# Optimization experiments

Measured on AMD Instinct MI355X. Metric: run time of the kernel, lower is better.

Reference implementation:

```python
import jax, jax.numpy as jnp
import numpy as np

B, S_SRC, S_TGT = 32, 128, 128
V, E, H = 32000, 256, 256
PAD_ID = 0
NEG = -1.0e9


def setup_inputs() -> dict:
    key = jax.random.key(0)
    ks = jax.random.split(key, 16)
    lengths_de = jax.random.randint(ks[0], (B,), S_SRC // 2, S_SRC + 1)
    idx_de = jax.random.randint(ks[1], (B, S_SRC), 1, V)
    pos = jnp.arange(S_SRC)[None, :]
    indices_de = jnp.where(pos < lengths_de[:, None], idx_de, PAD_ID)
    indices_en = jax.random.randint(ks[2], (B, S_TGT), 1, V)
    lengths_en = jnp.full((B,), S_TGT, dtype=jnp.int32)

    sc = 0.02
    def nrm(k, shape):
        return jax.random.normal(k, shape, dtype=jnp.float32) * sc
    emb_enc = nrm(ks[3], (V, E)).at[PAD_ID].set(0.0)
    emb_dec = nrm(ks[4], (V, E)).at[PAD_ID].set(0.0)
    return {
        "indices_de": indices_de, "lengths_de": lengths_de,
        "indices_en": indices_en, "lengths_en": lengths_en,
        "emb_enc": emb_enc, "emb_dec": emb_dec,
        "W_ih_enc": nrm(ks[5], (H, E)), "W_hh_enc": nrm(ks[6], (H, H)),
        "b_ih_enc": jnp.zeros((H,), jnp.float32), "b_hh_enc": jnp.zeros((H,), jnp.float32),
        "W_ih_dec": nrm(ks[7], (H, E)), "W_hh_dec": nrm(ks[8], (H, H)),
        "b_ih_dec": jnp.zeros((H,), jnp.float32), "b_hh_dec": jnp.zeros((H,), jnp.float32),
        "W_attn": nrm(ks[9], (H, 2 * H)), "b_attn": jnp.zeros((H,), jnp.float32),
        "W_out": nrm(ks[10], (V, H)), "b_out": jnp.zeros((V,), jnp.float32),
    }


def reference(indices_de, lengths_de, indices_en, lengths_en,
              emb_enc, emb_dec,
              W_ih_enc, W_hh_enc, b_ih_enc, b_hh_enc,
              W_ih_dec, W_hh_dec, b_ih_dec, b_hh_dec,
              W_attn, b_attn, W_out, b_out):
    # ---- Encoder: tanh RNN over packed sequence ----
    x_enc = emb_enc[indices_de]                      # [B, S, E]
    valid = jnp.arange(S_SRC)[None, :] < lengths_de[:, None]  # [B, S]

    def enc_step(h, inp):
        x_t, v_t = inp                                # [B,E], [B]
        h_new = jnp.tanh(x_t @ W_ih_enc.T + b_ih_enc + h @ W_hh_enc.T + b_hh_enc)
        h = jnp.where(v_t[:, None], h_new, h)         # frozen past length (pack semantics)
        out = jnp.where(v_t[:, None], h_new, 0.0)     # padded outputs are zero
        return h, out

    h0 = jnp.zeros((B, H), jnp.float32)
    h_final, enc_outs = jax.lax.scan(
        enc_step, h0, (x_enc.transpose(1, 0, 2), valid.T))
    encoder_outputs = enc_outs.transpose(1, 0, 2)     # [B, S, H]
    enc_mask = indices_de == PAD_ID                   # [B, S] True at padding

    # ---- Decoder: per-step RNN cell + dot-product attention + vocab proj ----
    x_dec = emb_dec[indices_en]                       # [B, T, E]

    def dec_step(h, x_t):
        h = jnp.tanh(x_t @ W_ih_dec.T + b_ih_dec + h @ W_hh_dec.T + b_hh_dec)
        scores = jnp.einsum('bh,bsh->bs', h, encoder_outputs)
        scores = jnp.where(enc_mask, NEG, scores)
        attn = jax.nn.softmax(scores, axis=-1)
        context = jnp.einsum('bs,bsh->bh', attn, encoder_outputs)
        combined = jnp.concatenate([context, h], axis=1)          # [B, 2H]
        attn_out = jnp.tanh(combined @ W_attn.T + b_attn)         # [B, H]
        logits_t = attn_out @ W_out.T + b_out                     # [B, V]
        return h, logits_t

    _, logits = jax.lax.scan(dec_step, h_final, x_dec.transpose(1, 0, 2))
    return logits.transpose(1, 0, 2)                  # [B, T, V]
```

## Files before the change

### kernel.cpp

```cpp
#include <hip/hip_runtime.h>
#include <stdint.h>

#define B_ 32
#define S_ 128
#define T_ 128
#define V_ 32000
#define E_ 256
#define H_ 256
#define NEG_ (-1.0e9f)

typedef __attribute__((ext_vector_type(8))) short short8;
typedef __attribute__((ext_vector_type(4))) float floatx4;

__device__ __forceinline__ unsigned short f2bf(float x){
  unsigned u = __float_as_uint(x);
  u = u + 0x7fffu + ((u >> 16) & 1u);
  return (unsigned short)(u >> 16);
}
__device__ __forceinline__ float bf2f(unsigned short s){
  return __uint_as_float(((unsigned)s) << 16);
}
__device__ __forceinline__ float hsum4(float4 v){ return (v.x+v.y)+(v.z+v.w); }
__device__ __forceinline__ void unpack8(uint4 q, float4& lo, float4& hi){
  lo.x = __uint_as_float(q.x << 16); lo.y = __uint_as_float(q.x & 0xffff0000u);
  lo.z = __uint_as_float(q.y << 16); lo.w = __uint_as_float(q.y & 0xffff0000u);
  hi.x = __uint_as_float(q.z << 16); hi.y = __uint_as_float(q.z & 0xffff0000u);
  hi.z = __uint_as_float(q.w << 16); hi.w = __uint_as_float(q.w & 0xffff0000u);
}

#define GLOAD_LDS16(gptr, lptr) \
  __builtin_amdgcn_global_load_lds( \
      (const __attribute__((address_space(1))) unsigned int*)(const void*)(gptr), \
      (__attribute__((address_space(3))) unsigned int*)(void*)(lptr), 16, 0, 0)

#define LDS_BARRIER() do { \
    asm volatile("s_waitcnt lgkmcnt(0)" ::: "memory"); \
    __builtin_amdgcn_s_barrier(); \
  } while(0)

__device__ __forceinline__ void cvt_body(const float* __restrict__ src,
                                         unsigned short* __restrict__ dst,
                                         int blk, int n4){
  int i = blk*256 + (int)threadIdx.x;
  if (i < n4){
    float4 v = ((const float4*)src)[i];
    ushort4 o; o.x=f2bf(v.x); o.y=f2bf(v.y); o.z=f2bf(v.z); o.w=f2bf(v.w);
    ((ushort4*)dst)[i] = o;
  }
}

__device__ __forceinline__ void xih_body(
    const int* __restrict__ idxmat, const float* __restrict__ emb,
    const float* __restrict__ Wih,
    const float* __restrict__ b1, const float* __restrict__ b2,
    float* __restrict__ out, int blk,
    int* idx_s, float4 (*x_s)[64])
{
  int b = blk >> 3;
  int t0 = (blk & 7) << 4;
  int tid = threadIdx.x;
  if (tid < 16) idx_s[tid] = idxmat[b*128 + t0 + tid];
  __syncthreads();
  for (int r = 0; r < 16; ++r)
    ((float*)&x_s[r][0])[tid] = emb[(size_t)idx_s[r]*E_ + tid];
  __syncthreads();
  int j2 = tid & 127, tg = tid >> 7;
  const float4* W0 = (const float4*)(Wih + (size_t)j2*E_);
  const float4* W1 = (const float4*)(Wih + (size_t)(j2+128)*E_);
  float4 a0[8], a1[8];
  #pragma unroll
  for (int t=0;t<8;++t){ a0[t]={0,0,0,0}; a1[t]={0,0,0,0}; }
  for (int e4 = 0; e4 < 64; ++e4){
    float4 w0 = W0[e4], w1 = W1[e4];
    #pragma unroll
    for (int t = 0; t < 8; ++t){
      float4 xv = x_s[tg*8+t][e4];
      a0[t] += w0*xv; a1[t] += w1*xv;
    }
  }
  float bi0 = b1[j2] + b2[j2];
  float bi1 = b1[j2+128] + b2[j2+128];
  #pragma unroll
  for (int t = 0; t < 8; ++t){
    size_t row = (size_t)((b<<7) + t0 + tg*8 + t)*H_;
    out[row + j2]     = hsum4(a0[t]) + bi0;
    out[row + j2+128] = hsum4(a1[t]) + bi1;
  }
}

__global__ __launch_bounds__(256) void k_prep(
    const float* __restrict__ W_out, unsigned short* __restrict__ Wout_bf,
    const float* __restrict__ W_attn, unsigned short* __restrict__ Wattn_bf,
    const int* __restrict__ indices_de, const float* __restrict__ emb_enc,
    const float* __restrict__ W_ih_enc, const float* __restrict__ b_ih_enc,
    const float* __restrict__ b_hh_enc, float* __restrict__ Xih_enc,
    const int* __restrict__ indices_en, const float* __restrict__ emb_dec,
    const float* __restrict__ W_ih_dec, const float* __restrict__ b_ih_dec,
    const float* __restrict__ b_hh_dec, float* __restrict__ Xih_dec)
{
  __shared__ int idx_s[16];
  __shared__ float4 x_s[16][64];
  int bx = blockIdx.x;
  if (bx < 8000){
    cvt_body(W_out, Wout_bf, bx, 2048000);
  } else if (bx < 8128){
    cvt_body(W_attn, Wattn_bf, bx - 8000, 32768);
  } else if (bx < 8384){
    xih_body(indices_de, emb_enc, W_ih_enc, b_ih_enc, b_hh_enc, Xih_enc,
             bx - 8128, idx_s, x_s);
  } else {
    xih_body(indices_en, emb_dec, W_ih_dec, b_ih_dec, b_hh_dec, Xih_dec,
             bx - 8384, idx_s, x_s);
  }
}

__global__ __launch_bounds__(512, 2) void k_rnn2(
    const float* __restrict__ Whh_e, const float* __restrict__ Whh_d,
    const float* __restrict__ Xih_e, const float* __restrict__ Xih_d,
    const int* __restrict__ lengths,
    unsigned short* __restrict__ enc_out,
    float* __restrict__ hseq)
{
  __shared__ float h_s[256];
  __shared__ float part[8][256];
  int b = blockIdx.x, tid = threadIdx.x;
  int kk = tid >> 6;
  int jg = tid & 63;
  float4 w[4][8];
  #pragma unroll
  for (int r = 0; r < 4; ++r){
    const float4* Wr = (const float4*)(Whh_e + (size_t)(jg + (r<<6))*H_ + (kk<<5));
    #pragma unroll
    for (int i = 0; i < 8; ++i) w[r][i] = Wr[i];
  }
  if (tid < 256) h_s[tid] = 0.f;
  int len = lengths[b];
  __syncthreads();

  for (int t = 0; t < 128; ++t){
    float x = 0.f;
    if (tid < 256) x = Xih_e[(size_t)((b<<7) + t)*H_ + tid];
    const float4* h4 = ((const float4*)h_s) + (kk << 3);
    float4 hv[8];
    #pragma unroll
    for (int i = 0; i < 8; ++i) hv[i] = h4[i];
    #pragma unroll
    for (int r = 0; r < 4; ++r){
      float4 a = {0,0,0,0};
      #pragma unroll
      for (int i = 0; i < 8; ++i) a += w[r][i]*hv[i];
      part[kk][jg + (r<<6)] = hsum4(a);
    }
    LDS_BARRIER();
    if (tid < 256){
      float s = x;
      #pragma unroll
      for (int q = 0; q < 8; ++q) s += part[q][tid];
      float hn = tanhf(s);
      float hold = h_s[tid];
      bool v = (t < len);
      h_s[tid] = v ? hn : hold;
      enc_out[(size_t)((b<<7)+t)*H_ + tid] = f2bf(v ? hn : 0.f);
    }
    LDS_BARRIER();
  }

  #pragma unroll
  for (int r = 0; r < 4; ++r){
    const float4* Wr = (const float4*)(Whh_d + (size_t)(jg + (r<<6))*H_ + (kk<<5));
    #pragma unroll
    for (int i = 0; i < 8; ++i) w[r][i] = Wr[i];
  }
  for (int t = 0; t < 128; ++t){
    float x = 0.f;
    if (tid < 256) x = Xih_d[(size_t)((b<<7) + t)*H_ + tid];
    const float4* h4 = ((const float4*)h_s) + (kk << 3);
    float4 hv[8];
    #pragma unroll
    for (int i = 0; i < 8; ++i) hv[i] = h4[i];
    #pragma unroll
    for (int r = 0; r < 4; ++r){
      float4 a = {0,0,0,0};
      #pragma unroll
      for (int i = 0; i < 8; ++i) a += w[r][i]*hv[i];
      part[kk][jg + (r<<6)] = hsum4(a);
    }
    LDS_BARRIER();
    if (tid < 256){
      float s = x;
      #pragma unroll
      for (int q = 0; q < 8; ++q) s += part[q][tid];
      float hn = tanhf(s);
      h_s[tid] = hn;
      hseq[(size_t)((b<<7)+t)*H_ + tid] = hn;
    }
    LDS_BARRIER();
  }
}

__global__ __launch_bounds__(256) void k_attn(
    const unsigned short* __restrict__ enc_out,
    const float* __restrict__ hseq,
    const int* __restrict__ lengths,
    const unsigned short* __restrict__ Wattn,
    const float* __restrict__ battn,
    unsigned short* __restrict__ attn_out)
{
  __shared__ float h_sm[16][256];
  __shared__ float sc[16][132];
  __shared__ float comb[16][512];
  int bx = blockIdx.x; int b = bx >> 3; int t0 = (bx & 7) << 4;
  int tid = threadIdx.x;
  int len = lengths[b];
  for (int r = 0; r < 16; ++r)
    h_sm[r][tid] = hseq[(size_t)((b<<7) + t0 + r)*H_ + tid];
  __syncthreads();
  {
    int s = tid & 127, tg = tid >> 7;
    float4 a[8];
    #pragma unroll
    for (int t=0;t<8;++t) a[t] = {0,0,0,0};
    const uint4* ep = (const uint4*)(enc_out + (size_t)(b*S_ + s)*H_);
    for (int oct = 0; oct < 32; ++oct){
      uint4 q = ep[oct];
      float4 elo, ehi; unpack8(q, elo, ehi);
      #pragma unroll
      for (int t = 0; t < 8; ++t){
        const float4* hp = (const float4*)&h_sm[tg*8+t][oct*8];
        a[t] += elo*hp[0] + ehi*hp[1];
      }
    }
    #pragma unroll
    for (int t = 0; t < 8; ++t)
      sc[tg*8+t][s] = (s < len) ? hsum4(a[t]) : NEG_;
  }
  __syncthreads();
  {
    int wv = tid >> 6, ln = tid & 63;
    for (int r = 0; r < 4; ++r){
      int t = r*4 + wv;
      float v0 = sc[t][ln], v1 = sc[t][ln+64];
      float m = fmaxf(v0, v1);
      #pragma unroll
      for (int off = 32; off >= 1; off >>= 1) m = fmaxf(m, __shfl_xor(m, off));
      float e0 = __expf(v0 - m), e1 = __expf(v1 - m);
      float su = e0 + e1;
      #pragma unroll
      for (int off = 32; off >= 1; off >>= 1) su += __shfl_xor(su, off);
      float inv = 1.0f / su;
      sc[t][ln] = e0*inv; sc[t][ln+64] = e1*inv;
    }
  }
  __syncthreads();
  {
    int hd = tid & 127, tg = tid >> 7;
    float c0[8], c1[8];
    #pragma unroll
    for (int t=0;t<8;++t){ c0[t]=0.f; c1[t]=0.f; }
    for (int s4 = 0; s4 < 32; ++s4){
      float ea[4], eb[4];
      #pragma unroll
      for (int i = 0; i < 4; ++i){
        const unsigned short* er = enc_out + (size_t)(b*S_ + s4*4 + i)*H_;
        ea[i] = bf2f(er[hd]); eb[i] = bf2f(er[hd+128]);
      }
      #pragma unroll
      for (int t = 0; t < 8; ++t){
        float4 av = *(const float4*)&sc[tg*8+t][s4*4];
        c0[t] += av.x*ea[0] + av.y*ea[1] + av.z*ea[2] + av.w*ea[3];
        c1[t] += av.x*eb[0] + av.y*eb[1] + av.z*eb[2] + av.w*eb[3];
      }
    }
    #pragma unroll
    for (int t = 0; t < 8; ++t){
      comb[tg*8+t][hd]     = c0[t];
      comb[tg*8+t][hd+128] = c1[t];
    }
  }
  for (int r = 0; r < 16; ++r) comb[r][256 + tid] = h_sm[r][tid];
  __syncthreads();
  {
    int j2 = tid & 127, tg = tid >> 7;
    float4 a0[8], a1[8];
    #pragma unroll
    for (int t=0;t<8;++t){ a0[t]={0,0,0,0}; a1[t]={0,0,0,0}; }
    const uint4* W0 = (const uint4*)(Wattn + (size_t)j2*512);
    const uint4* W1 = (const uint4*)(Wattn + (size_t)(j2+128)*512);
    for (int oct = 0; oct < 64; ++oct){
      float4 w0lo, w0hi, w1lo, w1hi;
      unpack8(W0[oct], w0lo, w0hi);
      unpack8(W1[oct], w1lo, w1hi);
      #pragma unroll
      for (int t = 0; t < 8; ++t){
        const float4* cp = (const float4*)&comb[tg*8+t][oct*8];
        float4 clo = cp[0], chi = cp[1];
        a0[t] += w0lo*clo + w0hi*chi;
        a1[t] += w1lo*clo + w1hi*chi;
      }
    }
    float bi0 = battn[j2], bi1 = battn[j2+128];
    #pragma unroll
    for (int t = 0; t < 8; ++t){
      size_t row = (size_t)((b<<7) + t0 + tg*8 + t)*H_;
      attn_out[row + j2]     = f2bf(tanhf(hsum4(a0[t]) + bi0));
      attn_out[row + j2+128] = f2bf(tanhf(hsum4(a1[t]) + bi1));
    }
  }
}

#define VB_STAGE(bufi, s) do { \
    _Pragma("unroll") \
    for (int i_ = 0; i_ < 4; ++i_){ \
      int c_ = tid + i_*512; \
      int r_ = c_ >> 5; \
      int sc_ = (c_ & 31) ^ (r_ & 7); \
      GLOAD_LDS16(Wb + (size_t)(ncol0 + (s)*64 + r_)*256 + sc_*8, \
                  &Bsm[bufi][c_*8]); \
    } \
  } while(0)

#define VB_STEP(s, Wlit, DOSTAGE) do { \
    asm volatile("s_waitcnt vmcnt(" Wlit ")" ::: "memory"); \
    __builtin_amdgcn_s_barrier(); \
    floatx4 acc[2][4]; \
    _Pragma("unroll") \
    for (int mi=0;mi<2;++mi) \
      _Pragma("unroll") \
      for (int ni=0;ni<4;++ni) acc[mi][ni]=(floatx4){0.f,0.f,0.f,0.f}; \
    _Pragma("unroll") \
    for (int k0=0;k0<8;++k0){ \
      short8 bfr[4]; \
      _Pragma("unroll") \
      for (int ni=0;ni<4;++ni) \
        bfr[ni] = *(const short8*)&Bsm[(s)&1][(ni*16+llo)*256 + (((k0*4+lhi)^(llo&7))<<3)]; \
      _Pragma("unroll") \
      for (int ni=0;ni<4;++ni){ \
        acc[0][ni] = __builtin_amdgcn_mfma_f32_16x16x32_bf16(af[0][k0], bfr[ni], acc[0][ni], 0,0,0); \
        acc[1][ni] = __builtin_amdgcn_mfma_f32_16x16x32_bf16(af[1][k0], bfr[ni], acc[1][ni], 0,0,0); \
      } \
    } \
    asm volatile("s_waitcnt lgkmcnt(0)" ::: "memory"); \
    __builtin_amdgcn_s_barrier(); \
    _Pragma("unroll") \
    for (int ni=0;ni<4;++ni){ \
      int col_ = ncol0 + (s)*64 + ni*16 + llo; \
      _Pragma("unroll") \
      for (int mi=0;mi<2;++mi){ \
        _Pragma("unroll") \
        for (int r_=0;r_<4;++r_){ \
          int row_ = mrow0 + mi*16 + lhi*4 + r_; \
          out[(size_t)row_*V_ + col_] = acc[mi][ni][r_] + bpre[s][ni]; \
        } \
      } \
    } \
    asm volatile("" ::: "memory"); \
    if (DOSTAGE) VB_STAGE((s)&1, (s)+2); \
    asm volatile("" ::: "memory"); \
  } while(0)

__global__ __launch_bounds__(512) void k_vocab(
    const unsigned short* __restrict__ A,
    const unsigned short* __restrict__ Wb,
    const float* __restrict__ bout,
    float* __restrict__ out)
{
  __shared__ alignas(16) unsigned short Bsm[2][64*256];
  int bid = blockIdx.x;
  int xcd = bid & 7;
  int gid = xcd*250 + (bid >> 3);
  int mb = gid / 125, ng = gid % 125;
  int tid = threadIdx.x;
  int ln  = tid & 63;
  int w   = tid >> 6;
  int llo = ln & 15, lhi = ln >> 4;
  int mrow0 = mb*256 + w*32;
  int ncol0 = ng*256;

  short8 af[2][8];
  #pragma unroll
  for (int mi=0;mi<2;++mi)
    #pragma unroll
    for (int k0=0;k0<8;++k0)
      af[mi][k0] = *(const short8*)(A + (size_t)(mrow0 + mi*16 + llo)*256 + k0*32 + lhi*8);
  float bpre[4][4];
  #pragma unroll
  for (int s=0;s<4;++s)
    #pragma unroll
    for (int ni=0;ni<4;++ni)
      bpre[s][ni] = bout[ncol0 + s*64 + ni*16 + llo];

  VB_STAGE(0, 0);
  VB_STAGE(1, 1);

  VB_STEP(0, "4",  1);
  VB_STEP(1, "36", 1);
  VB_STEP(2, "36", 0);
  VB_STEP(3, "32", 0);
}

extern "C" void kernel_launch(void* const* d_in, const int* in_sizes, int n_in,
                              void* d_out, int out_size, void* d_ws, size_t ws_size,
                              hipStream_t stream){
  const int*   indices_de = (const int*)d_in[0];
  const int*   lengths_de = (const int*)d_in[1];
  const int*   indices_en = (const int*)d_in[2];
  const float* emb_enc   = (const float*)d_in[4];
  const float* emb_dec   = (const float*)d_in[5];
  const float* W_ih_enc  = (const float*)d_in[6];
  const float* W_hh_enc  = (const float*)d_in[7];
  const float* b_ih_enc  = (const float*)d_in[8];
  const float* b_hh_enc  = (const float*)d_in[9];
  const float* W_ih_dec  = (const float*)d_in[10];
  const float* W_hh_dec  = (const float*)d_in[11];
  const float* b_ih_dec  = (const float*)d_in[12];
  const float* b_hh_dec  = (const float*)d_in[13];
  const float* W_attn    = (const float*)d_in[14];
  const float* b_attn    = (const float*)d_in[15];
  const float* W_out     = (const float*)d_in[16];
  const float* b_out     = (const float*)d_in[17];

  char* ws = (char*)d_ws;
  size_t o = 0;
  float* Xih_enc = (float*)(ws + o); o += (size_t)4096*256*4;
  float* Xih_dec = (float*)(ws + o); o += (size_t)4096*256*4;
  unsigned short* enc_bf = (unsigned short*)(ws + o); o += (size_t)4096*256*2;
  float* hdec    = (float*)(ws + o); o += (size_t)4096*256*4;
  unsigned short* attn_o  = (unsigned short*)(ws + o); o += (size_t)4096*256*2;
  unsigned short* Wout_bf = (unsigned short*)(ws + o); o += (size_t)V_*256*2;
  unsigned short* Wattn_bf= (unsigned short*)(ws + o); o += (size_t)256*512*2;

  k_prep<<<8640, 256, 0, stream>>>(
      W_out, Wout_bf, W_attn, Wattn_bf,
      indices_de, emb_enc, W_ih_enc, b_ih_enc, b_hh_enc, Xih_enc,
      indices_en, emb_dec, W_ih_dec, b_ih_dec, b_hh_dec, Xih_dec);
  k_rnn2<<<32, 512, 0, stream>>>(W_hh_enc, W_hh_dec, Xih_enc, Xih_dec,
                                 lengths_de, enc_bf, hdec);
  k_attn<<<256, 256, 0, stream>>>(enc_bf, hdec, lengths_de, Wattn_bf, b_attn, attn_o);
  k_vocab<<<2000, 512, 0, stream>>>(attn_o, Wout_bf, b_out, (float*)d_out);
}
```

Before: 943.9 us.

## Overlap weight bf16 conversion with serial RNN and vectorize vocab stores

Moves the W_out and W_attn fp32-to-bf16 conversion out of the prep kernel and into extra blocks of the RNN kernel. The 32 latency-bound recurrence blocks then run alongside the bandwidth-bound conversion instead of after it. The RNN inner loops are changed so each thread owns four contiguous output rows and writes its partial sums and h as vectors. The vocab GEMM swaps the MFMA operands so each lane holds four consecutive columns, which allows float4 output and bias accesses, and the vmcnt waits are adjusted to the new store count. The risk is that the conversion blocks compete with the recurrence blocks for CU time or bandwidth.

```diff
diff --git a/kernel.cpp b/kernel.cpp
--- a/kernel.cpp
+++ b/kernel.cpp
@@ -37,17 +37,6 @@
     asm volatile("s_waitcnt lgkmcnt(0)" ::: "memory"); \
     __builtin_amdgcn_s_barrier(); \
   } while(0)
-
-__device__ __forceinline__ void cvt_body(const float* __restrict__ src,
-                                         unsigned short* __restrict__ dst,
-                                         int blk, int n4){
-  int i = blk*256 + (int)threadIdx.x;
-  if (i < n4){
-    float4 v = ((const float4*)src)[i];
-    ushort4 o; o.x=f2bf(v.x); o.y=f2bf(v.y); o.z=f2bf(v.z); o.w=f2bf(v.w);
-    ((ushort4*)dst)[i] = o;
-  }
-}
 
 __device__ __forceinline__ void xih_body(
     const int* __restrict__ idxmat, const float* __restrict__ emb,
@@ -88,9 +77,7 @@
   }
 }
 
-__global__ __launch_bounds__(256) void k_prep(
-    const float* __restrict__ W_out, unsigned short* __restrict__ Wout_bf,
-    const float* __restrict__ W_attn, unsigned short* __restrict__ Wattn_bf,
+__global__ __launch_bounds__(256) void k_xih(
     const int* __restrict__ indices_de, const float* __restrict__ emb_enc,
     const float* __restrict__ W_ih_enc, const float* __restrict__ b_ih_enc,
     const float* __restrict__ b_hh_enc, float* __restrict__ Xih_enc,
@@ -101,35 +88,48 @@
   __shared__ int idx_s[16];
   __shared__ float4 x_s[16][64];
   int bx = blockIdx.x;
-  if (bx < 8000){
-    cvt_body(W_out, Wout_bf, bx, 2048000);
-  } else if (bx < 8128){
-    cvt_body(W_attn, Wattn_bf, bx - 8000, 32768);
-  } else if (bx < 8384){
+  if (bx < 256)
     xih_body(indices_de, emb_enc, W_ih_enc, b_ih_enc, b_hh_enc, Xih_enc,
-             bx - 8128, idx_s, x_s);
-  } else {
+             bx, idx_s, x_s);
+  else
     xih_body(indices_en, emb_dec, W_ih_dec, b_ih_dec, b_hh_dec, Xih_dec,
-             bx - 8384, idx_s, x_s);
-  }
-}
-
-__global__ __launch_bounds__(512, 2) void k_rnn2(
+             bx - 256, idx_s, x_s);
+}
+
+__global__ __launch_bounds__(512, 1) void k_rnnfused(
     const float* __restrict__ Whh_e, const float* __restrict__ Whh_d,
     const float* __restrict__ Xih_e, const float* __restrict__ Xih_d,
     const int* __restrict__ lengths,
     unsigned short* __restrict__ enc_out,
-    float* __restrict__ hseq)
+    float* __restrict__ hseq,
+    const float* __restrict__ W_out, unsigned short* __restrict__ Wout_bf,
+    const float* __restrict__ W_attn, unsigned short* __restrict__ Wattn_bf)
 {
-  __shared__ float h_s[256];
-  __shared__ float part[8][256];
-  int b = blockIdx.x, tid = threadIdx.x;
+  int bx = blockIdx.x;
+  int tid = threadIdx.x;
+  if (bx >= 32){
+    int cb = bx - 32;
+    const float* src; unsigned short* dst; int n4;
+    if (cb < 4000){ src = W_out; dst = Wout_bf; n4 = 2048000; }
+    else          { src = W_attn; dst = Wattn_bf; n4 = 32768; cb -= 4000; }
+    int i = cb*512 + tid;
+    if (i < n4){
+      float4 v = ((const float4*)src)[i];
+      ushort4 o; o.x=f2bf(v.x); o.y=f2bf(v.y); o.z=f2bf(v.z); o.w=f2bf(v.w);
+      ((ushort4*)dst)[i] = o;
+    }
+    return;
+  }
+  __shared__ alignas(16) float h_s[256];
+  __shared__ alignas(16) float part[8][256];
+  int b = bx;
   int kk = tid >> 6;
   int jg = tid & 63;
+  int j0 = jg << 2;
   float4 w[4][8];
   #pragma unroll
   for (int r = 0; r < 4; ++r){
-    const float4* Wr = (const float4*)(Whh_e + (size_t)(jg + (r<<6))*H_ + (kk<<5));
+    const float4* Wr = (const float4*)(Whh_e + (size_t)(j0 + r)*H_ + (kk<<5));
     #pragma unroll
     for (int i = 0; i < 8; ++i) w[r][i] = Wr[i];
   }
@@ -138,61 +138,77 @@
   __syncthreads();
 
   for (int t = 0; t < 128; ++t){
-    float x = 0.f;
-    if (tid < 256) x = Xih_e[(size_t)((b<<7) + t)*H_ + tid];
+    float2 x2 = {0.f, 0.f};
+    if (tid < 128) x2 = *(const float2*)&Xih_e[(size_t)((b<<7) + t)*H_ + tid*2];
     const float4* h4 = ((const float4*)h_s) + (kk << 3);
     float4 hv[8];
     #pragma unroll
     for (int i = 0; i < 8; ++i) hv[i] = h4[i];
-    #pragma unroll
-    for (int r = 0; r < 4; ++r){
-      float4 a = {0,0,0,0};
-      #pragma unroll
-      for (int i = 0; i < 8; ++i) a += w[r][i]*hv[i];
-      part[kk][jg + (r<<6)] = hsum4(a);
-    }
+    float4 pr;
+    {
+      float4 a0={0,0,0,0}, a1={0,0,0,0}, a2={0,0,0,0}, a3={0,0,0,0};
+      #pragma unroll
+      for (int i = 0; i < 8; ++i){
+        a0 += w[0][i]*hv[i]; a1 += w[1][i]*hv[i];
+        a2 += w[2][i]*hv[i]; a3 += w[3][i]*hv[i];
+      }
+      pr.x = hsum4(a0); pr.y = hsum4(a1); pr.z = hsum4(a2); pr.w = hsum4(a3);
+    }
+    *(float4*)&part[kk][j0] = pr;
     LDS_BARRIER();
-    if (tid < 256){
-      float s = x;
-      #pragma unroll
-      for (int q = 0; q < 8; ++q) s += part[q][tid];
-      float hn = tanhf(s);
-      float hold = h_s[tid];
+    if (tid < 128){
+      float s0 = x2.x, s1 = x2.y;
+      #pragma unroll
+      for (int q = 0; q < 8; ++q){
+        float2 p = *(const float2*)&part[q][tid*2];
+        s0 += p.x; s1 += p.y;
+      }
+      float hn0 = tanhf(s0), hn1 = tanhf(s1);
+      float2 old = *(const float2*)&h_s[tid*2];
       bool v = (t < len);
-      h_s[tid] = v ? hn : hold;
-      enc_out[(size_t)((b<<7)+t)*H_ + tid] = f2bf(v ? hn : 0.f);
+      float2 nh; nh.x = v ? hn0 : old.x; nh.y = v ? hn1 : old.y;
+      *(float2*)&h_s[tid*2] = nh;
+      ushort2 ob; ob.x = f2bf(v ? hn0 : 0.f); ob.y = f2bf(v ? hn1 : 0.f);
+      *(ushort2*)&enc_out[(size_t)((b<<7)+t)*H_ + tid*2] = ob;
     }
     LDS_BARRIER();
   }
 
   #pragma unroll
   for (int r = 0; r < 4; ++r){
-    const float4* Wr = (const float4*)(Whh_d + (size_t)(jg + (r<<6))*H_ + (kk<<5));
+    const float4* Wr = (const float4*)(Whh_d + (size_t)(j0 + r)*H_ + (kk<<5));
     #pragma unroll
     for (int i = 0; i < 8; ++i) w[r][i] = Wr[i];
   }
   for (int t = 0; t < 128; ++t){
-    float x = 0.f;
-    if (tid < 256) x = Xih_d[(size_t)((b<<7) + t)*H_ + tid];
+    float2 x2 = {0.f, 0.f};
+    if (tid < 128) x2 = *(const float2*)&Xih_d[(size_t)((b<<7) + t)*H_ + tid*2];
     const float4* h4 = ((const float4*)h_s) + (kk << 3);
     float4 hv[8];
     #pragma unroll
     for (int i = 0; i < 8; ++i) hv[i] = h4[i];
-    #pragma unroll
-    for (int r = 0; r < 4; ++r){
-      float4 a = {0,0,0,0};
-      #pragma unroll
-      for (int i = 0; i < 8; ++i) a += w[r][i]*hv[i];
-      part[kk][jg + (r<<6)] = hsum4(a);
-    }
+    float4 pr;
+    {
+      float4 a0={0,0,0,0}, a1={0,0,0,0}, a2={0,0,0,0}, a3={0,0,0,0};
+      #pragma unroll
+      for (int i = 0; i < 8; ++i){
+        a0 += w[0][i]*hv[i]; a1 += w[1][i]*hv[i];
+        a2 += w[2][i]*hv[i]; a3 += w[3][i]*hv[i];
+      }
+      pr.x = hsum4(a0); pr.y = hsum4(a1); pr.z = hsum4(a2); pr.w = hsum4(a3);
+    }
+    *(float4*)&part[kk][j0] = pr;
     LDS_BARRIER();
-    if (tid < 256){
-      float s = x;
-      #pragma unroll
-      for (int q = 0; q < 8; ++q) s += part[q][tid];
-      float hn = tanhf(s);
-      h_s[tid] = hn;
-      hseq[(size_t)((b<<7)+t)*H_ + tid] = hn;
+    if (tid < 128){
+      float s0 = x2.x, s1 = x2.y;
+      #pragma unroll
+      for (int q = 0; q < 8; ++q){
+        float2 p = *(const float2*)&part[q][tid*2];
+        s0 += p.x; s1 += p.y;
+      }
+      float hn0 = tanhf(s0), hn1 = tanhf(s1);
+      *(float2*)&h_s[tid*2] = (float2){hn0, hn1};
+      *(float2*)&hseq[(size_t)((b<<7)+t)*H_ + tid*2] = (float2){hn0, hn1};
     }
     LDS_BARRIER();
   }
@@ -335,22 +351,24 @@
         bfr[ni] = *(const short8*)&Bsm[(s)&1][(ni*16+llo)*256 + (((k0*4+lhi)^(llo&7))<<3)]; \
       _Pragma("unroll") \
       for (int ni=0;ni<4;++ni){ \
-        acc[0][ni] = __builtin_amdgcn_mfma_f32_16x16x32_bf16(af[0][k0], bfr[ni], acc[0][ni], 0,0,0); \
-        acc[1][ni] = __builtin_amdgcn_mfma_f32_16x16x32_bf16(af[1][k0], bfr[ni], acc[1][ni], 0,0,0); \
+        acc[0][ni] = __builtin_amdgcn_mfma_f32_16x16x32_bf16(bfr[ni], af[0][k0], acc[0][ni], 0,0,0); \
+        acc[1][ni] = __builtin_amdgcn_mfma_f32_16x16x32_bf16(bfr[ni], af[1][k0], acc[1][ni], 0,0,0); \
       } \
     } \
     asm volatile("s_waitcnt lgkmcnt(0)" ::: "memory"); \
     __builtin_amdgcn_s_barrier(); \
     _Pragma("unroll") \
     for (int ni=0;ni<4;++ni){ \
-      int col_ = ncol0 + (s)*64 + ni*16 + llo; \
+      int col_ = ncol0 + (s)*64 + ni*16 + (lhi<<2); \
       _Pragma("unroll") \
       for (int mi=0;mi<2;++mi){ \
-        _Pragma("unroll") \
-        for (int r_=0;r_<4;++r_){ \
-          int row_ = mrow0 + mi*16 + lhi*4 + r_; \
-          out[(size_t)row_*V_ + col_] = acc[mi][ni][r_] + bpre[s][ni]; \
-        } \
+        int row_ = mrow0 + mi*16 + llo; \
+        float4 o_; \
+        o_.x = acc[mi][ni][0] + bpre4[s][ni].x; \
+        o_.y = acc[mi][ni][1] + bpre4[s][ni].y; \
+        o_.z = acc[mi][ni][2] + bpre4[s][ni].z; \
+        o_.w = acc[mi][ni][3] + bpre4[s][ni].w; \
+        *(float4*)&out[(size_t)row_*V_ + col_] = o_; \
       } \
     } \
     asm volatile("" ::: "memory"); \
@@ -382,20 +400,20 @@
     #pragma unroll
     for (int k0=0;k0<8;++k0)
       af[mi][k0] = *(const short8*)(A + (size_t)(mrow0 + mi*16 + llo)*256 + k0*32 + lhi*8);
-  float bpre[4][4];
+  float4 bpre4[4][4];
   #pragma unroll
   for (int s=0;s<4;++s)
     #pragma unroll
     for (int ni=0;ni<4;++ni)
-      bpre[s][ni] = bout[ncol0 + s*64 + ni*16 + llo];
+      bpre4[s][ni] = *(const float4*)&bout[ncol0 + s*64 + ni*16 + (lhi<<2)];
 
   VB_STAGE(0, 0);
   VB_STAGE(1, 1);
 
   VB_STEP(0, "4",  1);
-  VB_STEP(1, "36", 1);
-  VB_STEP(2, "36", 0);
-  VB_STEP(3, "32", 0);
+  VB_STEP(1, "12", 1);
+  VB_STEP(2, "12", 0);
+  VB_STEP(3, "8",  0);
 }
 
 extern "C" void kernel_launch(void* const* d_in, const int* in_sizes, int n_in,
@@ -429,12 +447,12 @@
   unsigned short* Wout_bf = (unsigned short*)(ws + o); o += (size_t)V_*256*2;
   unsigned short* Wattn_bf= (unsigned short*)(ws + o); o += (size_t)256*512*2;
 
-  k_prep<<<8640, 256, 0, stream>>>(
-      W_out, Wout_bf, W_attn, Wattn_bf,
+  k_xih<<<512, 256, 0, stream>>>(
       indices_de, emb_enc, W_ih_enc, b_ih_enc, b_hh_enc, Xih_enc,
       indices_en, emb_dec, W_ih_dec, b_ih_dec, b_hh_dec, Xih_dec);
-  k_rnn2<<<32, 512, 0, stream>>>(W_hh_enc, W_hh_dec, Xih_enc, Xih_dec,
-                                 lengths_de, enc_bf, hdec);
+  k_rnnfused<<<4096, 512, 0, stream>>>(
+      W_hh_enc, W_hh_dec, Xih_enc, Xih_dec, lengths_de, enc_bf, hdec,
+      W_out, Wout_bf, W_attn, Wattn_bf);
   k_attn<<<256, 256, 0, stream>>>(enc_bf, hdec, lengths_de, Wattn_bf, b_attn, attn_o);
   k_vocab<<<2000, 512, 0, stream>>>(attn_o, Wout_bf, b_out, (float*)d_out);
 }
```

Result: no change. 950.3 us (+0.7%).
